# Performance work log

Hardware: AMD Instinct MI355X
Metric: run time of the kernel (lower is better)

The kernel has to match this reference:

```python
import jax, jax.numpy as jnp
import numpy as np

# Acoustic FDTD constants (seistorch-style geometry)
NSHOTS, NT = 4, 512
NZ, NX = 256, 256
NRECS = 128
DT = 1e-3   # s
DH = 10.0   # m grid spacing


def setup_inputs() -> dict:
    key = jax.random.key(0)
    k1, k2, k3, k4, k5, k6 = jax.random.split(key, 6)
    x = jax.random.normal(k1, (NSHOTS, NT), dtype=jnp.float32)  # source wavelets
    # velocity model in [1500, 4000] m/s (CFL: dt*vmax/dh = 0.4 < stability limit)
    vp = 1500.0 + 2500.0 * jax.random.uniform(k2, (NZ, NX), dtype=jnp.float32)
    src_z = jax.random.randint(k3, (NSHOTS,), 0, NZ)
    src_x = jax.random.randint(k4, (NSHOTS,), 0, NX)
    rec_z = jax.random.randint(k5, (NSHOTS, NRECS), 0, NZ)
    rec_x = jax.random.randint(k6, (NSHOTS, NRECS), 0, NX)
    return {"x": x, "vp": vp, "src_z": src_z, "src_x": src_x,
            "rec_z": rec_z, "rec_x": rec_x}


def _laplacian(p):
    # 5-point stencil, zero Dirichlet boundary. p: (B, NZ, NX)
    pp = jnp.pad(p, ((0, 0), (1, 1), (1, 1)))
    return (pp[:, 2:, 1:-1] + pp[:, :-2, 1:-1]
            + pp[:, 1:-1, 2:] + pp[:, 1:-1, :-2]
            - 4.0 * p) / (DH * DH)


def reference(x, vp, src_z, src_x, rec_z, rec_x):
    shots = jnp.arange(NSHOTS)
    c2dt2 = (vp * DT) ** 2  # (NZ, NX), broadcast over shots

    def step(carry, wav_t):
        p_prev, p = carry
        # 2nd-order acoustic update (the PDE "cell")
        p_next = 2.0 * p - p_prev + c2dt2 * _laplacian(p)
        # source scatter-inject (super_source)
        p_next = p_next.at[shots, src_z, src_x].add(wav_t * DT * DT)
        # receiver gather (super_probes): (NSHOTS, NRECS)
        rec = p_next[shots[:, None], rec_z, rec_x]
        return (p, p_next), rec

    p0 = jnp.zeros((NSHOTS, NZ, NX), dtype=x.dtype)
    _, recs = jax.lax.scan(step, (p0, p0), x.T)  # recs: (NT, NSHOTS, NRECS)
    # (shots, time, receivers, n_receiver_types=1)
    return jnp.transpose(recs, (1, 0, 2))[..., None]
```

## Files before the change

kernel.cpp:

```cpp
#include <hip/hip_runtime.h>

#define NSHOTS 4
#define NT     512
#define NZ     256
#define NX     256
#define NRECS  128

static constexpr float DTf    = 0.001f;
static constexpr float INVDH2 = 1.0f / (10.0f * 10.0f);

#define KSTEPS 8
#define TILEZ  16
#define TILEX  32
#define RPT    4
#define NPAIRS 2
#define NWAVES 8
#define BLOCK  512
#define NTZ    16
#define NTX    8
#define NTILES (NSHOTS * NTZ * NTX)
#define NPHASE (NT / KSTEPS)
#define LSTRIDE 32

typedef float v2f __attribute__((ext_vector_type(2)));

__device__ __forceinline__ float nbr_left(float v) {
  return __int_as_float(__builtin_amdgcn_update_dpp(
      0, __float_as_int(v), 0x138 , 0xf, 0xf, true));
}
__device__ __forceinline__ float nbr_right(float v) {
  return __int_as_float(__builtin_amdgcn_update_dpp(
      0, __float_as_int(v), 0x130 , 0xf, 0xf, true));
}

__device__ __forceinline__ float gload(const float* p) {
  return __hip_atomic_load(p, __ATOMIC_RELAXED, __HIP_MEMORY_SCOPE_AGENT);
}
__device__ __forceinline__ void gstore(float* p, float v) {
  __hip_atomic_store(p, v, __ATOMIC_RELAXED, __HIP_MEMORY_SCOPE_AGENT);
}
__device__ __forceinline__ unsigned fload(const unsigned* p) {
  return __hip_atomic_load(p, __ATOMIC_RELAXED, __HIP_MEMORY_SCOPE_AGENT);
}
__device__ __forceinline__ void fstore(unsigned* p, unsigned v) {
  __hip_atomic_store(p, v, __ATOMIC_RELAXED, __HIP_MEMORY_SCOPE_AGENT);
}

__global__ __launch_bounds__(BLOCK, 4) void wave_pk(
    float* __restrict__ f0c, float* __restrict__ f0p,
    float* __restrict__ f1c, float* __restrict__ f1p,
    const float* __restrict__ vp, const float* __restrict__ xwav,
    const int* __restrict__ src_z, const int* __restrict__ src_x,
    const int* __restrict__ rec_z, const int* __restrict__ rec_x,
    float* __restrict__ out,
    unsigned* __restrict__ bar)
{
  const int bid  = blockIdx.x;
  const int s    = bid >> 7;
  const int tz   = (bid >> 3) & 15;
  const int tx   = bid & 7;
  const int tid  = threadIdx.x;
  const int w    = tid >> 6;
  const int lane = tid & 63;

  const int gz0 = tz * TILEZ - KSTEPS;
  const int gx0 = tx * TILEX - KSTEPS;
  const int gx  = gx0 + lane;
  const int zb  = w * RPT;

  __shared__ float haloTop[2][NWAVES][64];
  __shared__ float haloBot[2][NWAVES][64];
  __shared__ float recTile[2][TILEZ][TILEX + 1];
  __shared__ int   cntS;
  __shared__ int   lzA[NRECS], lxA[NRECS];
  __shared__ unsigned pkA[NRECS];

  if (tid == 0) cntS = 0;
  __syncthreads();
  if (tid < NRECS) {
    const int lz = rec_z[s * NRECS + tid] - tz * TILEZ;
    const int lx = rec_x[s * NRECS + tid] - tx * TILEX;
    lzA[tid] = lz; lxA[tid] = lx;
    if ((unsigned)lz < (unsigned)TILEZ && (unsigned)lx < (unsigned)TILEX) {
      const int k = atomicAdd(&cntS, 1);
      pkA[k] = (unsigned)tid | ((unsigned)lz << 8) | ((unsigned)lx << 16);
    }
  }
  __syncthreads();
  const int nRec = cntS;
  int myR = 0, myLz = 0, myLx = 0;
  if (tid < nRec) {
    const unsigned p = pkA[tid];
    myR = p & 255; myLz = (p >> 8) & 31; myLx = (p >> 16) & 31;
  }
  const bool wbRow = (w >= 2 && w < 6) && (lane >= KSTEPS && lane < KSTEPS + TILEX);
  const int  ilz   = (w - 2) * RPT;
  const int  ilx   = lane - KSTEPS;
  unsigned recMask = 0;
  if (wbRow) {
    for (int r = 0; r < NRECS; ++r)
      if (lxA[r] == ilx && (unsigned)(lzA[r] - ilz) < (unsigned)RPT)
        recMask |= 1u << (lzA[r] - ilz);
  }

  int nb = -1;
  if (tid < 8) {
    const int k  = (tid < 4) ? tid : tid + 1;
    const int dz = k / 3 - 1, dx = k % 3 - 1;
    const int qz = tz + dz, qx = tx + dx;
    if ((unsigned)qz < (unsigned)NTZ && (unsigned)qx < (unsigned)NTX)
      nb = (s << 7) | (qz << 3) | qx;
  }
  unsigned* wF = bar;

  auto pollGE = [&](unsigned* base, unsigned target) {
    if (nb >= 0) {
      while (fload(base + (size_t)nb * LSTRIDE) < target)
        __builtin_amdgcn_s_sleep(1);
    }
  };

  const int slz = src_z[s] - gz0;
  const int slx = src_x[s] - gx0;
  const bool srcMine = (slx == lane) && ((unsigned)(slz - zb) < (unsigned)RPT);
  const int  srcI = slz - zb;
  v2f srcM2[NPAIRS];
  #pragma unroll
  for (int p = 0; p < NPAIRS; ++p) {
    srcM2[p].x = (srcMine && srcI == 2 * p)     ? 1.0f : 0.0f;
    srcM2[p].y = (srcMine && srcI == 2 * p + 1) ? 1.0f : 0.0f;
  }

  const bool xok = (unsigned)gx < (unsigned)NX;
  int   offRow[RPT];
  bool  okRow[RPT];
  v2f a2[NPAIRS], b2[NPAIRS], c22[NPAIRS], d22[NPAIRS];
  #pragma unroll
  for (int p = 0; p < NPAIRS; ++p) {
    #pragma unroll
    for (int h = 0; h < 2; ++h) {
      const int i  = 2 * p + h;
      const int gz = gz0 + zb + i;
      const bool ok = xok && ((unsigned)gz < (unsigned)NZ);
      okRow[i]  = ok;
      offRow[i] = ok ? ((s * NZ + gz) * NX + gx) : 0;
      float v = ok ? vp[gz * NX + gx] : 0.0f;
      v *= DTf;
      const float c2 = v * v * INVDH2;
      if (h == 0) { c22[p].x = c2; d22[p].x = 2.0f - 4.0f * c2; }
      else        { c22[p].y = c2; d22[p].y = 2.0f - 4.0f * c2; }
    }
    a2[p] = (v2f)(0.0f); b2[p] = (v2f)(0.0f);
  }

  #pragma unroll 1
  for (int ph = 0; ph < NPHASE; ++ph) {
    const int t0 = ph * KSTEPS;

    float amp[KSTEPS];
    {
      const float4* xw4 = (const float4*)(xwav + s * NT + t0);
      #pragma unroll
      for (int q = 0; q < KSTEPS / 4; ++q) {
        const float4 v = xw4[q];
        amp[4 * q + 0] = (v.x * DTf) * DTf;
        amp[4 * q + 1] = (v.y * DTf) * DTf;
        amp[4 * q + 2] = (v.z * DTf) * DTf;
        amp[4 * q + 3] = (v.w * DTf) * DTf;
      }
    }

    if (ph > 0) {
      pollGE(wF, (unsigned)ph);
      __syncthreads();
      const float* rc = (ph & 1) ? f0c : f1c;
      const float* rp = (ph & 1) ? f0p : f1p;
      if (!wbRow) {
        #pragma unroll
        for (int p = 0; p < NPAIRS; ++p) {
          a2[p].x = okRow[2 * p]     ? gload(rc + offRow[2 * p])     : 0.0f;
          a2[p].y = okRow[2 * p + 1] ? gload(rc + offRow[2 * p + 1]) : 0.0f;
          b2[p].x = okRow[2 * p]     ? gload(rp + offRow[2 * p])     : 0.0f;
          b2[p].y = okRow[2 * p + 1] ? gload(rp + offRow[2 * p + 1]) : 0.0f;
        }
      }
    }

    float recv[KSTEPS];

    auto do_step = [&](v2f (&cur)[NPAIRS], v2f (&nxt)[NPAIRS], int tau) {
      const int pb = tau & 1;
      haloTop[pb][w][lane] = cur[0].x;
      haloBot[pb][w][lane] = cur[NPAIRS - 1].y;
      __syncthreads();
      if (tau > 0 && tid < nRec) recv[tau - 1] = recTile[1 - pb][myLz][myLx];
      const float up0 = (w > 0)          ? haloBot[pb][w - 1][lane] : 0.0f;
      const float dn7 = (w < NWAVES - 1) ? haloTop[pb][w + 1][lane] : 0.0f;
      const v2f av = { amp[tau], amp[tau] };
      #pragma unroll
      for (int p = 0; p < NPAIRS; ++p) {
        const float cx = cur[p].x, cy = cur[p].y;
        const float upx = (p == 0)          ? up0 : cur[p - 1].y;
        const float dny = (p == NPAIRS - 1) ? dn7 : cur[p + 1].x;
        v2f ud, lr;
        ud.x = upx + cy;
        ud.y = cx + dny;
        lr.x = nbr_left(cx) + nbr_right(cx);
        lr.y = nbr_left(cy) + nbr_right(cy);
        const v2f sum = ud + lr;
        v2f t = __builtin_elementwise_fma(c22[p], sum, -nxt[p]);
        t = __builtin_elementwise_fma(d22[p], cur[p], t);
        t = __builtin_elementwise_fma(srcM2[p], av, t);
        nxt[p] = t;
      }
      if (recMask) {
        #pragma unroll
        for (int i = 0; i < RPT; ++i)
          if (recMask & (1u << i))
            recTile[pb][ilz + i][ilx] = (i & 1) ? nxt[i >> 1].y : nxt[i >> 1].x;
      }
    };

    #pragma unroll
    for (int h = 0; h < KSTEPS / 2; ++h) {
      do_step(a2, b2, 2 * h);
      do_step(b2, a2, 2 * h + 1);
    }

    if (ph != NPHASE - 1) {
      float* wc = (ph & 1) ? f1c : f0c;
      float* wp = (ph & 1) ? f1p : f0p;
      if (wbRow) {
        #pragma unroll
        for (int p = 0; p < NPAIRS; ++p) {
          gstore(wc + offRow[2 * p],     a2[p].x);
          gstore(wc + offRow[2 * p + 1], a2[p].y);
          gstore(wp + offRow[2 * p],     b2[p].x);
          gstore(wp + offRow[2 * p + 1], b2[p].y);
        }
      }
      __builtin_amdgcn_s_waitcnt(0);
      __syncthreads();
      if (tid == 0) fstore(wF + (size_t)bid * LSTRIDE, (unsigned)(ph + 1));
    } else {
      __syncthreads();
    }

    if (tid < nRec) {
      recv[KSTEPS - 1] = recTile[1][myLz][myLx];
      #pragma unroll
      for (int t = 0; t < KSTEPS; ++t)
        out[(s * NT + (t0 + t)) * NRECS + myR] = recv[t];
    }
  }
}

extern "C" void kernel_launch(void* const* d_in, const int* in_sizes, int n_in,
                              void* d_out, int out_size, void* d_ws, size_t ws_size,
                              hipStream_t stream) {
  const float* x     = (const float*)d_in[0];
  const float* vp    = (const float*)d_in[1];
  const int*   src_z = (const int*)d_in[2];
  const int*   src_x = (const int*)d_in[3];
  const int*   rec_z = (const int*)d_in[4];
  const int*   rec_x = (const int*)d_in[5];
  float* out = (float*)d_out;

  float* ws = (float*)d_ws;
  const size_t F = (size_t)NSHOTS * NZ * NX;
  float* f0c = ws;
  float* f0p = ws + F;
  float* f1c = ws + 2 * F;
  float* f1p = ws + 3 * F;
  unsigned* bar = (unsigned*)(ws + 4 * F);

  hipMemsetAsync(bar, 0, (size_t)NTILES * LSTRIDE * sizeof(unsigned), stream);

  wave_pk<<<dim3(NTILES), dim3(BLOCK), 0, stream>>>(
      f0c, f0p, f1c, f1p, vp, x, src_z, src_x, rec_z, rec_x, out, bar);
}
```

Measured before the change: 323.2 us.

## Use single-wavefront tiles with register-resident z-column and direct receiver writes

Replaces the 512-thread blocks (8 wavefronts exchanging z-halos through LDS with a __syncthreads every step) with 64-thread single-wavefront blocks. Each lane holds a 24-row z column (8 interior rows plus 8 halo rows each side) in registers, so a step needs no barriers. The grid grows to 1024 tiles of 8x32 with 16-column x halos, and receivers are written straight to global memory from registers instead of being staged through LDS. The cost is much more redundant halo computation, more registers per lane, and more global halo loads per phase.

```diff
diff --git a/kernel.cpp b/kernel.cpp
--- a/kernel.cpp
+++ b/kernel.cpp
@@ -10,16 +10,15 @@
 static constexpr float INVDH2 = 1.0f / (10.0f * 10.0f);
 
 #define KSTEPS 8
-#define TILEZ  16
-#define TILEX  32
-#define RPT    4
-#define NPAIRS 2
-#define NWAVES 8
-#define BLOCK  512
-#define NTZ    16
-#define NTX    8
-#define NTILES (NSHOTS * NTZ * NTX)
-#define NPHASE (NT / KSTEPS)
+#define TZ     8
+#define XI     32
+#define HALOX  16
+#define EXTZ   (TZ + 2*KSTEPS)
+#define NPR    (EXTZ/2)
+#define NTZT   (NZ/TZ)
+#define NTXT   (NX/XI)
+#define NTILES (NSHOTS*NTZT*NTXT)
+#define NPHASE (NT/KSTEPS)
 #define LSTRIDE 32
 
 typedef float v2f __attribute__((ext_vector_type(2)));
@@ -46,7 +45,7 @@
   __hip_atomic_store(p, v, __ATOMIC_RELAXED, __HIP_MEMORY_SCOPE_AGENT);
 }
 
-__global__ __launch_bounds__(BLOCK, 4) void wave_pk(
+__global__ __launch_bounds__(64) void wave_pk(
     float* __restrict__ f0c, float* __restrict__ f0p,
     float* __restrict__ f1c, float* __restrict__ f1p,
     const float* __restrict__ vp, const float* __restrict__ xwav,
@@ -56,95 +55,30 @@
     unsigned* __restrict__ bar)
 {
   const int bid  = blockIdx.x;
-  const int s    = bid >> 7;
-  const int tz   = (bid >> 3) & 15;
+  const int s    = bid >> 8;
+  const int tz   = (bid >> 3) & 31;
   const int tx   = bid & 7;
-  const int tid  = threadIdx.x;
-  const int w    = tid >> 6;
-  const int lane = tid & 63;
-
-  const int gz0 = tz * TILEZ - KSTEPS;
-  const int gx0 = tx * TILEX - KSTEPS;
+  const int lane = threadIdx.x;
+
+  const int gz0 = tz * TZ - KSTEPS;
+  const int gx0 = tx * XI - HALOX;
   const int gx  = gx0 + lane;
-  const int zb  = w * RPT;
-
-  __shared__ float haloTop[2][NWAVES][64];
-  __shared__ float haloBot[2][NWAVES][64];
-  __shared__ float recTile[2][TILEZ][TILEX + 1];
-  __shared__ int   cntS;
-  __shared__ int   lzA[NRECS], lxA[NRECS];
-  __shared__ unsigned pkA[NRECS];
-
-  if (tid == 0) cntS = 0;
-  __syncthreads();
-  if (tid < NRECS) {
-    const int lz = rec_z[s * NRECS + tid] - tz * TILEZ;
-    const int lx = rec_x[s * NRECS + tid] - tx * TILEX;
-    lzA[tid] = lz; lxA[tid] = lx;
-    if ((unsigned)lz < (unsigned)TILEZ && (unsigned)lx < (unsigned)TILEX) {
-      const int k = atomicAdd(&cntS, 1);
-      pkA[k] = (unsigned)tid | ((unsigned)lz << 8) | ((unsigned)lx << 16);
-    }
-  }
-  __syncthreads();
-  const int nRec = cntS;
-  int myR = 0, myLz = 0, myLx = 0;
-  if (tid < nRec) {
-    const unsigned p = pkA[tid];
-    myR = p & 255; myLz = (p >> 8) & 31; myLx = (p >> 16) & 31;
-  }
-  const bool wbRow = (w >= 2 && w < 6) && (lane >= KSTEPS && lane < KSTEPS + TILEX);
-  const int  ilz   = (w - 2) * RPT;
-  const int  ilx   = lane - KSTEPS;
-  unsigned recMask = 0;
-  if (wbRow) {
-    for (int r = 0; r < NRECS; ++r)
-      if (lxA[r] == ilx && (unsigned)(lzA[r] - ilz) < (unsigned)RPT)
-        recMask |= 1u << (lzA[r] - ilz);
-  }
-
-  int nb = -1;
-  if (tid < 8) {
-    const int k  = (tid < 4) ? tid : tid + 1;
-    const int dz = k / 3 - 1, dx = k % 3 - 1;
-    const int qz = tz + dz, qx = tx + dx;
-    if ((unsigned)qz < (unsigned)NTZ && (unsigned)qx < (unsigned)NTX)
-      nb = (s << 7) | (qz << 3) | qx;
-  }
-  unsigned* wF = bar;
-
-  auto pollGE = [&](unsigned* base, unsigned target) {
-    if (nb >= 0) {
-      while (fload(base + (size_t)nb * LSTRIDE) < target)
-        __builtin_amdgcn_s_sleep(1);
-    }
-  };
-
-  const int slz = src_z[s] - gz0;
-  const int slx = src_x[s] - gx0;
-  const bool srcMine = (slx == lane) && ((unsigned)(slz - zb) < (unsigned)RPT);
-  const int  srcI = slz - zb;
-  v2f srcM2[NPAIRS];
+  const bool haloLane = (lane < HALOX) || (lane >= HALOX + XI);
+  const bool xok = (unsigned)gx < (unsigned)NX;
+  const int off0 = (s * NZ + gz0) * NX + gx;
+
+  unsigned okBits = 0;
   #pragma unroll
-  for (int p = 0; p < NPAIRS; ++p) {
-    srcM2[p].x = (srcMine && srcI == 2 * p)     ? 1.0f : 0.0f;
-    srcM2[p].y = (srcMine && srcI == 2 * p + 1) ? 1.0f : 0.0f;
-  }
-
-  const bool xok = (unsigned)gx < (unsigned)NX;
-  int   offRow[RPT];
-  bool  okRow[RPT];
-  v2f a2[NPAIRS], b2[NPAIRS], c22[NPAIRS], d22[NPAIRS];
+  for (int i = 0; i < EXTZ; ++i)
+    if (xok && (unsigned)(gz0 + i) < (unsigned)NZ) okBits |= 1u << i;
+
+  v2f c22[NPR], d22[NPR], a2[NPR], b2[NPR];
   #pragma unroll
-  for (int p = 0; p < NPAIRS; ++p) {
+  for (int p = 0; p < NPR; ++p) {
     #pragma unroll
     for (int h = 0; h < 2; ++h) {
-      const int i  = 2 * p + h;
-      const int gz = gz0 + zb + i;
-      const bool ok = xok && ((unsigned)gz < (unsigned)NZ);
-      okRow[i]  = ok;
-      offRow[i] = ok ? ((s * NZ + gz) * NX + gx) : 0;
-      float v = ok ? vp[gz * NX + gx] : 0.0f;
+      const int i = 2 * p + h;
+      float v = ((okBits >> i) & 1) ? vp[(gz0 + i) * NX + gx] : 0.0f;
       v *= DTf;
       const float c2 = v * v * INVDH2;
       if (h == 0) { c22[p].x = c2; d22[p].x = 2.0f - 4.0f * c2; }
@@ -153,104 +87,157 @@
     a2[p] = (v2f)(0.0f); b2[p] = (v2f)(0.0f);
   }
 
+  const int slz = src_z[s] - gz0;
+  const int slx = src_x[s] - gx0;
+  const bool hasSrc = ((unsigned)slz < (unsigned)EXTZ) &&
+                      ((unsigned)slx < 64u);
+  v2f srcM2[NPR];
+  #pragma unroll
+  for (int p = 0; p < NPR; ++p) {
+    srcM2[p].x = (slx == lane && slz == 2 * p)     ? 1.0f : 0.0f;
+    srcM2[p].y = (slx == lane && slz == 2 * p + 1) ? 1.0f : 0.0f;
+  }
+
+  const int gzi0 = tz * TZ;
+  unsigned e0 = 0, e1 = 0, rB0 = 0, rB1 = 0, rB2 = 0, rB3 = 0;
+  int cnt = 0;
+  #pragma unroll 1
+  for (int r = 0; r < NRECS; ++r) {
+    const int rz = rec_z[s * NRECS + r];
+    const int rx = rec_x[s * NRECS + r];
+    const int row = rz - gzi0;
+    if (!haloLane && rx == gx && (unsigned)row < (unsigned)TZ) {
+      const unsigned e = (unsigned)r | ((unsigned)row << 8) | 0x8000u;
+      if (cnt == 0) e0 = e;
+      else if (cnt == 1) e1 = e;
+      else {
+        if (r < 32)       rB0 |= 1u << r;
+        else if (r < 64)  rB1 |= 1u << (r - 32);
+        else if (r < 96)  rB2 |= 1u << (r - 64);
+        else              rB3 |= 1u << (r - 96);
+      }
+      ++cnt;
+    }
+  }
+  const bool hasOvf = (rB0 | rB1 | rB2 | rB3) != 0;
+
+  int nb = -1;
+  if (lane < 8) {
+    const int k  = (lane < 4) ? lane : lane + 1;
+    const int dz = k / 3 - 1, dx = k % 3 - 1;
+    const int qz = tz + dz, qx = tx + dx;
+    if ((unsigned)qz < (unsigned)NTZT && (unsigned)qx < (unsigned)NTXT)
+      nb = (s << 8) | (qz << 3) | qx;
+  }
+  unsigned* wF = bar;
+
+  float amp[KSTEPS];
+
+  auto selRow = [](const v2f (&n)[NPR], int row) -> float {
+    const int pr = row >> 1;
+    float vx = n[4].x, vy = n[4].y;
+    vx = (pr == 1) ? n[5].x : vx;  vy = (pr == 1) ? n[5].y : vy;
+    vx = (pr == 2) ? n[6].x : vx;  vy = (pr == 2) ? n[6].y : vy;
+    vx = (pr == 3) ? n[7].x : vx;  vy = (pr == 3) ? n[7].y : vy;
+    return (row & 1) ? vy : vx;
+  };
+
+  auto do_step = [&](v2f (&cur)[NPR], v2f (&nxt)[NPR], int tau, int t0) {
+    const v2f av = { amp[tau], amp[tau] };
+    #pragma unroll
+    for (int p = 0; p < NPR; ++p) {
+      const float cx = cur[p].x, cy = cur[p].y;
+      const float upx = (p == 0)       ? 0.0f : cur[p - 1].y;
+      const float dny = (p == NPR - 1) ? 0.0f : cur[p + 1].x;
+      v2f ud, lr;
+      ud.x = upx + cy;
+      ud.y = cx + dny;
+      lr.x = nbr_left(cx) + nbr_right(cx);
+      lr.y = nbr_left(cy) + nbr_right(cy);
+      const v2f sum = ud + lr;
+      v2f t = __builtin_elementwise_fma(c22[p], sum, -nxt[p]);
+      t = __builtin_elementwise_fma(d22[p], cur[p], t);
+      nxt[p] = t;
+    }
+    if (hasSrc) {
+      #pragma unroll
+      for (int p = 0; p < NPR; ++p)
+        nxt[p] = __builtin_elementwise_fma(srcM2[p], av, nxt[p]);
+    }
+    const int t = t0 + tau;
+    if (e0 & 0x8000u)
+      out[(s * NT + t) * NRECS + (e0 & 127u)] = selRow(nxt, (e0 >> 8) & 7);
+    if (e1 & 0x8000u)
+      out[(s * NT + t) * NRECS + (e1 & 127u)] = selRow(nxt, (e1 >> 8) & 7);
+    if (hasOvf) {
+      #pragma unroll
+      for (int wd = 0; wd < 4; ++wd) {
+        unsigned m = (wd == 0) ? rB0 : (wd == 1) ? rB1 : (wd == 2) ? rB2 : rB3;
+        while (m) {
+          const int b = __builtin_ctz(m); m &= m - 1;
+          const int r = wd * 32 + b;
+          const int row = rec_z[s * NRECS + r] - gzi0;
+          out[(s * NT + t) * NRECS + r] = selRow(nxt, row);
+        }
+      }
+    }
+  };
+
   #pragma unroll 1
   for (int ph = 0; ph < NPHASE; ++ph) {
     const int t0 = ph * KSTEPS;
 
-    float amp[KSTEPS];
     {
-      const float4* xw4 = (const float4*)(xwav + s * NT + t0);
-      #pragma unroll
-      for (int q = 0; q < KSTEPS / 4; ++q) {
-        const float4 v = xw4[q];
-        amp[4 * q + 0] = (v.x * DTf) * DTf;
-        amp[4 * q + 1] = (v.y * DTf) * DTf;
-        amp[4 * q + 2] = (v.z * DTf) * DTf;
-        amp[4 * q + 3] = (v.w * DTf) * DTf;
-      }
+      const float4 v = *(const float4*)(xwav + s * NT + t0);
+      const float4 w = *(const float4*)(xwav + s * NT + t0 + 4);
+      amp[0] = v.x * DTf * DTf; amp[1] = v.y * DTf * DTf;
+      amp[2] = v.z * DTf * DTf; amp[3] = v.w * DTf * DTf;
+      amp[4] = w.x * DTf * DTf; amp[5] = w.y * DTf * DTf;
+      amp[6] = w.z * DTf * DTf; amp[7] = w.w * DTf * DTf;
     }
 
     if (ph > 0) {
-      pollGE(wF, (unsigned)ph);
-      __syncthreads();
+      if (nb >= 0) {
+        while (fload(wF + (size_t)nb * LSTRIDE) < (unsigned)ph)
+          __builtin_amdgcn_s_sleep(1);
+      }
+      __asm__ volatile("" ::: "memory");
       const float* rc = (ph & 1) ? f0c : f1c;
       const float* rp = (ph & 1) ? f0p : f1p;
-      if (!wbRow) {
-        #pragma unroll
-        for (int p = 0; p < NPAIRS; ++p) {
-          a2[p].x = okRow[2 * p]     ? gload(rc + offRow[2 * p])     : 0.0f;
-          a2[p].y = okRow[2 * p + 1] ? gload(rc + offRow[2 * p + 1]) : 0.0f;
-          b2[p].x = okRow[2 * p]     ? gload(rp + offRow[2 * p])     : 0.0f;
-          b2[p].y = okRow[2 * p + 1] ? gload(rp + offRow[2 * p + 1]) : 0.0f;
+      #pragma unroll
+      for (int i = 0; i < EXTZ; ++i) {
+        const bool zHalo = (i < KSTEPS) || (i >= KSTEPS + TZ);
+        if (zHalo || haloLane) {
+          const bool ok = (okBits >> i) & 1;
+          const int off = off0 + i * NX;
+          const float cv = ok ? gload(rc + off) : 0.0f;
+          const float pv = ok ? gload(rp + off) : 0.0f;
+          if (i & 1) { a2[i >> 1].y = cv; b2[i >> 1].y = pv; }
+          else       { a2[i >> 1].x = cv; b2[i >> 1].x = pv; }
         }
       }
     }
 
-    float recv[KSTEPS];
-
-    auto do_step = [&](v2f (&cur)[NPAIRS], v2f (&nxt)[NPAIRS], int tau) {
-      const int pb = tau & 1;
-      haloTop[pb][w][lane] = cur[0].x;
-      haloBot[pb][w][lane] = cur[NPAIRS - 1].y;
-      __syncthreads();
-      if (tau > 0 && tid < nRec) recv[tau - 1] = recTile[1 - pb][myLz][myLx];
-      const float up0 = (w > 0)          ? haloBot[pb][w - 1][lane] : 0.0f;
-      const float dn7 = (w < NWAVES - 1) ? haloTop[pb][w + 1][lane] : 0.0f;
-      const v2f av = { amp[tau], amp[tau] };
-      #pragma unroll
-      for (int p = 0; p < NPAIRS; ++p) {
-        const float cx = cur[p].x, cy = cur[p].y;
-        const float upx = (p == 0)          ? up0 : cur[p - 1].y;
-        const float dny = (p == NPAIRS - 1) ? dn7 : cur[p + 1].x;
-        v2f ud, lr;
-        ud.x = upx + cy;
-        ud.y = cx + dny;
-        lr.x = nbr_left(cx) + nbr_right(cx);
-        lr.y = nbr_left(cy) + nbr_right(cy);
-        const v2f sum = ud + lr;
-        v2f t = __builtin_elementwise_fma(c22[p], sum, -nxt[p]);
-        t = __builtin_elementwise_fma(d22[p], cur[p], t);
-        t = __builtin_elementwise_fma(srcM2[p], av, t);
-        nxt[p] = t;
-      }
-      if (recMask) {
-        #pragma unroll
-        for (int i = 0; i < RPT; ++i)
-          if (recMask & (1u << i))
-            recTile[pb][ilz + i][ilx] = (i & 1) ? nxt[i >> 1].y : nxt[i >> 1].x;
-      }
-    };
-
     #pragma unroll
-    for (int h = 0; h < KSTEPS / 2; ++h) {
-      do_step(a2, b2, 2 * h);
-      do_step(b2, a2, 2 * h + 1);
+    for (int hh = 0; hh < KSTEPS / 2; ++hh) {
+      do_step(a2, b2, 2 * hh,     t0);
+      do_step(b2, a2, 2 * hh + 1, t0);
     }
 
     if (ph != NPHASE - 1) {
       float* wc = (ph & 1) ? f1c : f0c;
       float* wp = (ph & 1) ? f1p : f0p;
-      if (wbRow) {
+      if (!haloLane) {
         #pragma unroll
-        for (int p = 0; p < NPAIRS; ++p) {
-          gstore(wc + offRow[2 * p],     a2[p].x);
-          gstore(wc + offRow[2 * p + 1], a2[p].y);
-          gstore(wp + offRow[2 * p],     b2[p].x);
-          gstore(wp + offRow[2 * p + 1], b2[p].y);
+        for (int i = KSTEPS; i < KSTEPS + TZ; ++i) {
+          const int off = off0 + i * NX;
+          gstore(wc + off, (i & 1) ? a2[i >> 1].y : a2[i >> 1].x);
+          gstore(wp + off, (i & 1) ? b2[i >> 1].y : b2[i >> 1].x);
         }
       }
+      __asm__ volatile("" ::: "memory");
       __builtin_amdgcn_s_waitcnt(0);
-      __syncthreads();
-      if (tid == 0) fstore(wF + (size_t)bid * LSTRIDE, (unsigned)(ph + 1));
-    } else {
-      __syncthreads();
-    }
-
-    if (tid < nRec) {
-      recv[KSTEPS - 1] = recTile[1][myLz][myLx];
-      #pragma unroll
-      for (int t = 0; t < KSTEPS; ++t)
-        out[(s * NT + (t0 + t)) * NRECS + myR] = recv[t];
+      if (lane == 0) fstore(wF + (size_t)bid * LSTRIDE, (unsigned)(ph + 1));
     }
   }
 }
@@ -276,6 +263,6 @@
 
   hipMemsetAsync(bar, 0, (size_t)NTILES * LSTRIDE * sizeof(unsigned), stream);
 
-  wave_pk<<<dim3(NTILES), dim3(BLOCK), 0, stream>>>(
+  wave_pk<<<dim3(NTILES), dim3(64), 0, stream>>>(
       f0c, f0p, f1c, f1p, vp, x, src_z, src_x, rec_z, rec_x, out, bar);
 }
```

New measurement: 450.0 us. +39.2%, slower.
